# Kernel optimization log

Hardware: AMD Instinct MI355X
Metric: run time of the kernel (lower is better)

## Reference

```python
import jax, jax.numpy as jnp
import numpy as np

EPS = 1e-8  # torch.nn.CosineSimilarity default eps


def setup_inputs() -> dict:
    key = jax.random.key(0)
    ks = jax.random.split(key, 6)
    B, N, SD, HD, AD = 512, 256, 1024, 512, 256
    return {
        "state_emb": jax.random.normal(ks[0], (B, SD), dtype=jnp.float32),
        "hints_emb": jax.random.normal(ks[1], (B, N, HD), dtype=jnp.float32),
        "Ws": jax.random.normal(ks[2], (AD, SD), dtype=jnp.float32) * 0.02,
        "bs": jax.random.normal(ks[3], (AD,), dtype=jnp.float32) * 0.02,
        "Wh": jax.random.normal(ks[4], (AD, HD), dtype=jnp.float32) * 0.02,
        "bh": jax.random.normal(ks[5], (AD,), dtype=jnp.float32) * 0.02,
    }


def reference(state_emb, hints_emb, Ws, bs, Wh, bh):
    # Projections
    sp = state_emb @ Ws.T + bs                       # (B, A)
    hp = jnp.einsum("bnh,ah->bna", hints_emb, Wh) + bh  # (B, N, A)
    # Cosine similarity along feature dim (torch CosineSimilarity semantics)
    sn = jnp.maximum(jnp.linalg.norm(sp, axis=-1, keepdims=True), EPS)    # (B,1)
    hn = jnp.maximum(jnp.linalg.norm(hp, axis=-1), EPS)                   # (B,N)
    scores = jnp.einsum("ba,bna->bn", sp, hp) / (sn * hn)                 # (B,N)
    attn_weights = jax.nn.softmax(scores, axis=1)                         # (B,N)
    # Weighted sum over hints (original, unprojected embeddings)
    output = jnp.einsum("bn,bnh->bh", attn_weights, hints_emb)            # (B,HD)
    return output
```

## Files before the change

### kernel.cpp

```cpp
#include <hip/hip_runtime.h>
#include <hip/hip_bf16.h>

typedef __attribute__((ext_vector_type(8))) short bf16x8;
typedef __attribute__((ext_vector_type(4))) float f32x4;

#define B_  512
#define N_  256
#define SD_ 1024
#define HD_ 512
#define AD_ 256

__device__ __forceinline__ unsigned short f2bf(float f) {
    unsigned int u = __float_as_uint(f);
    unsigned int r = (u + 0x7FFFu + ((u >> 16) & 1u)) >> 16;
    return (unsigned short)r;
}

__global__ void k0_pack(const float* __restrict__ Wh, unsigned short* __restrict__ whp) {
    int g = blockIdx.x * 256 + threadIdx.x;
    int ct  = g >> 10;
    int rem = g & 1023;
    int ks  = rem >> 6;
    int l   = rem & 63;
    int a   = ct * 16 + (l & 15);
    int kb  = ks * 32 + (l >> 4) * 8;
    const float* src = Wh + (size_t)a * HD_ + kb;
    float4 v0 = *(const float4*)(src);
    float4 v1 = *(const float4*)(src + 4);
    bf16x8 o;
    o[0] = (short)f2bf(v0.x); o[1] = (short)f2bf(v0.y);
    o[2] = (short)f2bf(v0.z); o[3] = (short)f2bf(v0.w);
    o[4] = (short)f2bf(v1.x); o[5] = (short)f2bf(v1.y);
    o[6] = (short)f2bf(v1.z); o[7] = (short)f2bf(v1.w);
    ((bf16x8*)whp)[g] = o;
}

__global__ __launch_bounds__(512) void k1_proj(
    const float* __restrict__ state, const float* __restrict__ Ws,
    const float* __restrict__ bs,
    float* __restrict__ sn, float* __restrict__ spv)
{
    __shared__ float st[2][SD_];
    __shared__ float spl[2][AD_];
    __shared__ float red[2][AD_];
    int tid = threadIdx.x, lane = tid & 63, w = tid >> 6;
    int b0 = blockIdx.x * 2;
    ((float4*)st)[tid] = ((const float4*)(state + (size_t)b0 * SD_))[tid];
    __syncthreads();
    float4 s0[4], s1[4];
    #pragma unroll
    for (int seg = 0; seg < 4; ++seg) {
        s0[seg] = *(const float4*)&st[0][seg * 256 + lane * 4];
        s1[seg] = *(const float4*)&st[1][seg * 256 + lane * 4];
    }
    #pragma unroll 2
    for (int i = 0; i < 32; ++i) {
        int a = w * 32 + i;
        const float4* wr = (const float4*)(Ws + (size_t)a * SD_);
        float p0 = 0.f, p1 = 0.f;
        #pragma unroll
        for (int seg = 0; seg < 4; ++seg) {
            float4 wv = wr[seg * 64 + lane];
            p0 += wv.x * s0[seg].x + wv.y * s0[seg].y + wv.z * s0[seg].z + wv.w * s0[seg].w;
            p1 += wv.x * s1[seg].x + wv.y * s1[seg].y + wv.z * s1[seg].z + wv.w * s1[seg].w;
        }
        #pragma unroll
        for (int d = 1; d < 64; d <<= 1) { p0 += __shfl_xor(p0, d); p1 += __shfl_xor(p1, d); }
        if (lane == 0) {
            float bsa = bs[a];
            spl[0][a] = p0 + bsa;
            spl[1][a] = p1 + bsa;
        }
    }
    __syncthreads();
    int tb = tid >> 8, t = tid & 255;
    float sv = spl[tb][t];
    spv[(size_t)(b0 + tb) * AD_ + t] = sv;
    red[tb][t] = sv * sv;
    __syncthreads();
    for (int s = 128; s > 0; s >>= 1) { if (t < s) red[tb][t] += red[tb][t + s]; __syncthreads(); }
    if (t == 0) sn[b0 + tb] = fmaxf(sqrtf(red[tb][0]), 1e-8f);
}

__device__ __forceinline__ void stage_tile(unsigned short* buf, const float4* v,
                                           int rr, int cg) {
    #pragma unroll
    for (int j = 0; j < 4; ++j) {
        int row = j * 16 + rr;
        float4 x = v[j];
        ushort4 u;
        u.x = f2bf(x.x); u.y = f2bf(x.y); u.z = f2bf(x.z); u.w = f2bf(x.w);
        *(ushort4*)((char*)buf + row * 256 + ((cg * 8) ^ ((row & 7) << 4))) = u;
    }
}

__global__ __launch_bounds__(512, 2) void k2_fused(
    const float* __restrict__ hints, const unsigned short* __restrict__ whp,
    const float* __restrict__ spv, const float* __restrict__ sn,
    const float* __restrict__ bh, float* __restrict__ out)
{
    __shared__ __align__(16) char smem[41984];
    unsigned short* A_bf0 = (unsigned short*)smem;
    unsigned short* A_bf1 = (unsigned short*)(smem + 16384);
    float* sp_lds  = (float*)(smem + 32768);
    float* bh_lds  = (float*)(smem + 33792);
    float* norm2p  = (float*)(smem + 34816);
    float* nump    = (float*)(smem + 36864);
    float* sc      = (float*)(smem + 38912);
    float* red     = (float*)(smem + 39936);
    float* wsm     = (float*)(smem + 40960);
    float* scratch = (float*)smem;

    int tid = threadIdx.x, lane = tid & 63, w = tid >> 6;
    int b = blockIdx.x;
    const float* hb = hints + (size_t)b * N_ * HD_;
    if (tid < 64) ((float4*)sp_lds)[tid] = ((const float4*)(spv + (size_t)b * AD_))[tid];
    else if (tid < 128) ((float4*)bh_lds)[tid - 64] = ((const float4*)bh)[tid - 64];
    float snb = sn[b];
    int rr = tid >> 5;
    int cg = tid & 31;
    int cl = lane & 15;
    const float* hrow = hb + (size_t)rr * HD_ + cg * 4;
    __syncthreads();
    float bh0 = bh_lds[(2 * w + 0) * 16 + cl];
    float bh1 = bh_lds[(2 * w + 1) * 16 + cl];
    float sp0 = sp_lds[(2 * w + 0) * 16 + cl];
    float sp1 = sp_lds[(2 * w + 1) * 16 + cl];

    float4 v[4];
    #pragma unroll
    for (int j = 0; j < 4; ++j)
        v[j] = *(const float4*)(hrow + (size_t)(j * 16) * HD_);

    for (int mc = 0; mc < 4; ++mc) {
        f32x4 acc[4][2];
        #pragma unroll
        for (int mf = 0; mf < 4; ++mf) {
            acc[mf][0] = (f32x4){0.f, 0.f, 0.f, 0.f};
            acc[mf][1] = (f32x4){0.f, 0.f, 0.f, 0.f};
        }
        stage_tile(A_bf0, v, rr, cg);
        __syncthreads();

        for (int kc = 0; kc < 4; ++kc) {
            if (kc < 3) {
                #pragma unroll
                for (int j = 0; j < 4; ++j)
                    v[j] = *(const float4*)(hrow + (size_t)(mc * 64 + j * 16) * HD_ + (kc + 1) * 128);
            }
            const unsigned short* Ab = (kc & 1) ? A_bf1 : A_bf0;
            int kc4 = kc * 4;
            #pragma unroll
            for (int ks = 0; ks < 4; ++ks) {
                bf16x8 bfr0 = ((const bf16x8*)whp)[((2 * w + 0) * 16 + kc4 + ks) * 64 + lane];
                bf16x8 bfr1 = ((const bf16x8*)whp)[((2 * w + 1) * 16 + kc4 + ks) * 64 + lane];
                #pragma unroll
                for (int mf = 0; mf < 4; ++mf) {
                    int r = mf * 16 + cl;
                    bf16x8 afr = *(const bf16x8*)((const char*)Ab + r * 256 +
                                 ((ks * 64 + (lane >> 4) * 16) ^ ((r & 7) << 4)));
                    acc[mf][0] = __builtin_amdgcn_mfma_f32_16x16x32_bf16(afr, bfr0, acc[mf][0], 0, 0, 0);
                    acc[mf][1] = __builtin_amdgcn_mfma_f32_16x16x32_bf16(afr, bfr1, acc[mf][1], 0, 0, 0);
                }
            }
            if (kc < 3) stage_tile((kc & 1) ? A_bf0 : A_bf1, v, rr, cg);
            __syncthreads();
        }

        #pragma unroll
        for (int mf = 0; mf < 4; ++mf) {
            #pragma unroll
            for (int r = 0; r < 4; ++r) {
                float h0 = acc[mf][0][r] + bh0;
                float h1 = acc[mf][1][r] + bh1;
                float vv = h0 * h0 + h1 * h1;
                float uu = sp0 * h0 + sp1 * h1;
                vv += __shfl_xor(vv, 1); uu += __shfl_xor(uu, 1);
                vv += __shfl_xor(vv, 2); uu += __shfl_xor(uu, 2);
                vv += __shfl_xor(vv, 4); uu += __shfl_xor(uu, 4);
                vv += __shfl_xor(vv, 8); uu += __shfl_xor(uu, 8);
                if (cl == 0) {
                    int idx = w * 64 + mf * 16 + (lane >> 4) * 4 + r;
                    norm2p[idx] = vv;
                    nump[idx]   = uu;
                }
            }
        }
        if (mc < 3) {
            #pragma unroll
            for (int j = 0; j < 4; ++j)
                v[j] = *(const float4*)(hrow + (size_t)((mc + 1) * 64 + j * 16) * HD_);
        }
        __syncthreads();
        if (tid < 64) {
            float n2 = 0.f, nm = 0.f;
            #pragma unroll
            for (int ww = 0; ww < 8; ++ww) {
                n2 += norm2p[ww * 64 + tid];
                nm += nump[ww * 64 + tid];
            }
            float hn = fmaxf(sqrtf(n2), 1e-8f);
            sc[mc * 64 + tid] = nm / (snb * hn);
        }
        __syncthreads();
    }

    if (tid < 256) red[tid] = sc[tid];
    __syncthreads();
    for (int s = 128; s > 0; s >>= 1) { if (tid < s) red[tid] = fmaxf(red[tid], red[tid + s]); __syncthreads(); }
    float mx = red[0];
    __syncthreads();
    if (tid < 256) { float e = __expf(sc[tid] - mx); sc[tid] = e; red[tid] = e; }
    __syncthreads();
    for (int s = 128; s > 0; s >>= 1) { if (tid < s) red[tid] += red[tid + s]; __syncthreads(); }
    float inv = 1.f / red[0];
    __syncthreads();
    if (tid < 256) wsm[tid] = sc[tid] * inv;
    __syncthreads();

    int hg = tid & 127, ng = tid >> 7;
    const float* hbe = hb + (size_t)(ng * 64) * HD_ + hg * 4;
    float ax = 0.f, ay = 0.f, az = 0.f, aw = 0.f;
    #pragma unroll 8
    for (int n = 0; n < 64; ++n) {
        float4 hv = *(const float4*)(hbe + (size_t)n * HD_);
        float wn = wsm[ng * 64 + n];
        ax += wn * hv.x; ay += wn * hv.y; az += wn * hv.z; aw += wn * hv.w;
    }
    *(float4*)(scratch + ng * 512 + hg * 4) = (float4){ax, ay, az, aw};
    __syncthreads();
    out[(size_t)b * HD_ + tid] =
        scratch[tid] + scratch[512 + tid] + scratch[1024 + tid] + scratch[1536 + tid];
}

extern "C" void kernel_launch(void* const* d_in, const int* in_sizes, int n_in,
                              void* d_out, int out_size, void* d_ws, size_t ws_size,
                              hipStream_t stream) {
    const float* state = (const float*)d_in[0];
    const float* hints = (const float*)d_in[1];
    const float* Ws    = (const float*)d_in[2];
    const float* bs    = (const float*)d_in[3];
    const float* Wh    = (const float*)d_in[4];
    const float* bh    = (const float*)d_in[5];
    float* out = (float*)d_out;

    float* sn = (float*)d_ws;
    float* spv = sn + B_;
    unsigned short* whp = (unsigned short*)(spv + (size_t)B_ * AD_);

    k0_pack<<<64, 256, 0, stream>>>(Wh, whp);
    k1_proj<<<B_ / 2, 512, 0, stream>>>(state, Ws, bs, sn, spv);
    k2_fused<<<B_, 512, 0, stream>>>(hints, whp, spv, sn, bh, out);
}
```

Measured before the change: 153.2 us.

## Triple-buffer LDS tiles with two-stage register prefetch across chunk boundaries

```diff
diff --git a/kernel.cpp b/kernel.cpp
--- a/kernel.cpp
+++ b/kernel.cpp
@@ -90,7 +90,7 @@
         float4 x = v[j];
         ushort4 u;
         u.x = f2bf(x.x); u.y = f2bf(x.y); u.z = f2bf(x.z); u.w = f2bf(x.w);
-        *(ushort4*)((char*)buf + row * 256 + ((cg * 8) ^ ((row & 7) << 4))) = u;
+        *(ushort4*)((char*)buf + row * 256 + ((cg * 8) ^ ((row & 15) << 4))) = u;
     }
 }
 
@@ -99,16 +99,17 @@
     const float* __restrict__ spv, const float* __restrict__ sn,
     const float* __restrict__ bh, float* __restrict__ out)
 {
-    __shared__ __align__(16) char smem[41984];
-    unsigned short* A_bf0 = (unsigned short*)smem;
-    unsigned short* A_bf1 = (unsigned short*)(smem + 16384);
-    float* sp_lds  = (float*)(smem + 32768);
-    float* bh_lds  = (float*)(smem + 33792);
-    float* norm2p  = (float*)(smem + 34816);
-    float* nump    = (float*)(smem + 36864);
-    float* sc      = (float*)(smem + 38912);
-    float* red     = (float*)(smem + 39936);
-    float* wsm     = (float*)(smem + 40960);
+    __shared__ __align__(16) char smem[58368];
+    unsigned short* buf0 = (unsigned short*)smem;
+    unsigned short* buf1 = (unsigned short*)(smem + 16384);
+    unsigned short* buf2 = (unsigned short*)(smem + 32768);
+    float* sp_lds  = (float*)(smem + 49152);
+    float* bh_lds  = (float*)(smem + 50176);
+    float* norm2p  = (float*)(smem + 51200);
+    float* nump    = (float*)(smem + 53248);
+    float* sc      = (float*)(smem + 55296);
+    float* red     = (float*)(smem + 56320);
+    float* wsm     = (float*)(smem + 57344);
     float* scratch = (float*)smem;
 
     int tid = threadIdx.x, lane = tid & 63, w = tid >> 6;
@@ -127,10 +128,16 @@
     float sp0 = sp_lds[(2 * w + 0) * 16 + cl];
     float sp1 = sp_lds[(2 * w + 1) * 16 + cl];
 
-    float4 v[4];
-    #pragma unroll
-    for (int j = 0; j < 4; ++j)
-        v[j] = *(const float4*)(hrow + (size_t)(j * 16) * HD_);
+#define LADDR(p, j) (hrow + (size_t)(((p) >> 2) * 64 + (j) * 16) * HD_ + ((p) & 3) * 128)
+
+    float4 va[4], vb[4];
+    #pragma unroll
+    for (int j = 0; j < 4; ++j) va[j] = *(const float4*)LADDR(0, j);
+    #pragma unroll
+    for (int j = 0; j < 4; ++j) vb[j] = *(const float4*)LADDR(1, j);
+    stage_tile(buf0, va, rr, cg);
+    __syncthreads();
+    unsigned short *bufR = buf0, *bufW = buf1, *bufS = buf2;
 
     for (int mc = 0; mc < 4; ++mc) {
         f32x4 acc[4][2];
@@ -139,32 +146,34 @@
             acc[mf][0] = (f32x4){0.f, 0.f, 0.f, 0.f};
             acc[mf][1] = (f32x4){0.f, 0.f, 0.f, 0.f};
         }
-        stage_tile(A_bf0, v, rr, cg);
-        __syncthreads();
-
+        #pragma unroll
         for (int kc = 0; kc < 4; ++kc) {
-            if (kc < 3) {
-                #pragma unroll
-                for (int j = 0; j < 4; ++j)
-                    v[j] = *(const float4*)(hrow + (size_t)(mc * 64 + j * 16) * HD_ + (kc + 1) * 128);
-            }
-            const unsigned short* Ab = (kc & 1) ? A_bf1 : A_bf0;
-            int kc4 = kc * 4;
+            int p = mc * 4 + kc;
+            if (p + 2 < 16) {
+                if ((kc & 1) == 0) {
+                    #pragma unroll
+                    for (int j = 0; j < 4; ++j) va[j] = *(const float4*)LADDR(p + 2, j);
+                } else {
+                    #pragma unroll
+                    for (int j = 0; j < 4; ++j) vb[j] = *(const float4*)LADDR(p + 2, j);
+                }
+            }
             #pragma unroll
             for (int ks = 0; ks < 4; ++ks) {
-                bf16x8 bfr0 = ((const bf16x8*)whp)[((2 * w + 0) * 16 + kc4 + ks) * 64 + lane];
-                bf16x8 bfr1 = ((const bf16x8*)whp)[((2 * w + 1) * 16 + kc4 + ks) * 64 + lane];
+                bf16x8 bfr0 = ((const bf16x8*)whp)[((2 * w + 0) * 16 + kc * 4 + ks) * 64 + lane];
+                bf16x8 bfr1 = ((const bf16x8*)whp)[((2 * w + 1) * 16 + kc * 4 + ks) * 64 + lane];
                 #pragma unroll
                 for (int mf = 0; mf < 4; ++mf) {
                     int r = mf * 16 + cl;
-                    bf16x8 afr = *(const bf16x8*)((const char*)Ab + r * 256 +
-                                 ((ks * 64 + (lane >> 4) * 16) ^ ((r & 7) << 4)));
+                    bf16x8 afr = *(const bf16x8*)((const char*)bufR + r * 256 +
+                                 ((ks * 64 + (lane >> 4) * 16) ^ ((r & 15) << 4)));
                     acc[mf][0] = __builtin_amdgcn_mfma_f32_16x16x32_bf16(afr, bfr0, acc[mf][0], 0, 0, 0);
                     acc[mf][1] = __builtin_amdgcn_mfma_f32_16x16x32_bf16(afr, bfr1, acc[mf][1], 0, 0, 0);
                 }
             }
-            if (kc < 3) stage_tile((kc & 1) ? A_bf0 : A_bf1, v, rr, cg);
+            if (p + 1 < 16) stage_tile(bufW, (kc & 1) ? va : vb, rr, cg);
             __syncthreads();
+            unsigned short* t0 = bufR; bufR = bufW; bufW = bufS; bufS = t0;
         }
 
         #pragma unroll
@@ -186,11 +195,6 @@
                 }
             }
         }
-        if (mc < 3) {
-            #pragma unroll
-            for (int j = 0; j < 4; ++j)
-                v[j] = *(const float4*)(hrow + (size_t)((mc + 1) * 64 + j * 16) * HD_);
-        }
         __syncthreads();
         if (tid < 64) {
             float n2 = 0.f, nm = 0.f;
@@ -204,6 +208,7 @@
         }
         __syncthreads();
     }
+#undef LADDR
 
     if (tid < 256) red[tid] = sc[tid];
     __syncthreads();
```

New measurement: 147.6 us. 3.7% less time.

## Stage full 64x512 bf16 hint tile per chunk instead of double-buffered K slices

Applied to the files above, without the earlier changes.

```diff
diff --git a/kernel.cpp b/kernel.cpp
--- a/kernel.cpp
+++ b/kernel.cpp
@@ -82,33 +82,20 @@
     if (t == 0) sn[b0 + tb] = fmaxf(sqrtf(red[tb][0]), 1e-8f);
 }
 
-__device__ __forceinline__ void stage_tile(unsigned short* buf, const float4* v,
-                                           int rr, int cg) {
-    #pragma unroll
-    for (int j = 0; j < 4; ++j) {
-        int row = j * 16 + rr;
-        float4 x = v[j];
-        ushort4 u;
-        u.x = f2bf(x.x); u.y = f2bf(x.y); u.z = f2bf(x.z); u.w = f2bf(x.w);
-        *(ushort4*)((char*)buf + row * 256 + ((cg * 8) ^ ((row & 7) << 4))) = u;
-    }
-}
-
 __global__ __launch_bounds__(512, 2) void k2_fused(
     const float* __restrict__ hints, const unsigned short* __restrict__ whp,
     const float* __restrict__ spv, const float* __restrict__ sn,
     const float* __restrict__ bh, float* __restrict__ out)
 {
-    __shared__ __align__(16) char smem[41984];
-    unsigned short* A_bf0 = (unsigned short*)smem;
-    unsigned short* A_bf1 = (unsigned short*)(smem + 16384);
-    float* sp_lds  = (float*)(smem + 32768);
-    float* bh_lds  = (float*)(smem + 33792);
-    float* norm2p  = (float*)(smem + 34816);
-    float* nump    = (float*)(smem + 36864);
-    float* sc      = (float*)(smem + 38912);
-    float* red     = (float*)(smem + 39936);
-    float* wsm     = (float*)(smem + 40960);
+    __shared__ __align__(16) char smem[74752];
+    unsigned short* tile = (unsigned short*)smem;
+    float* sp_lds  = (float*)(smem + 65536);
+    float* bh_lds  = (float*)(smem + 66560);
+    float* norm2p  = (float*)(smem + 67584);
+    float* nump    = (float*)(smem + 69632);
+    float* sc      = (float*)(smem + 71680);
+    float* red     = (float*)(smem + 72704);
+    float* wsm     = (float*)(smem + 73728);
     float* scratch = (float*)smem;
 
     int tid = threadIdx.x, lane = tid & 63, w = tid >> 6;
@@ -117,54 +104,59 @@
     if (tid < 64) ((float4*)sp_lds)[tid] = ((const float4*)(spv + (size_t)b * AD_))[tid];
     else if (tid < 128) ((float4*)bh_lds)[tid - 64] = ((const float4*)bh)[tid - 64];
     float snb = sn[b];
-    int rr = tid >> 5;
-    int cg = tid & 31;
     int cl = lane & 15;
-    const float* hrow = hb + (size_t)rr * HD_ + cg * 4;
+    int srow = tid >> 3;
+    int sseg = tid & 7;
+    const float* srcrow = hb + (size_t)srow * HD_ + sseg * 64;
     __syncthreads();
     float bh0 = bh_lds[(2 * w + 0) * 16 + cl];
     float bh1 = bh_lds[(2 * w + 1) * 16 + cl];
     float sp0 = sp_lds[(2 * w + 0) * 16 + cl];
     float sp1 = sp_lds[(2 * w + 1) * 16 + cl];
 
-    float4 v[4];
-    #pragma unroll
-    for (int j = 0; j < 4; ++j)
-        v[j] = *(const float4*)(hrow + (size_t)(j * 16) * HD_);
-
+    #pragma unroll 1
     for (int mc = 0; mc < 4; ++mc) {
+        const float* src = srcrow + (size_t)(mc * 64) * HD_;
+        #pragma unroll
+        for (int h = 0; h < 2; ++h) {
+            float4 v[8];
+            #pragma unroll
+            for (int j = 0; j < 8; ++j)
+                v[j] = *(const float4*)(src + h * 32 + j * 4);
+            #pragma unroll
+            for (int j2 = 0; j2 < 4; ++j2) {
+                int s = sseg * 8 + h * 4 + j2;
+                int sw = s ^ (srow & 15);
+                float4 a = v[2 * j2], c = v[2 * j2 + 1];
+                bf16x8 pk;
+                pk[0] = (short)f2bf(a.x); pk[1] = (short)f2bf(a.y);
+                pk[2] = (short)f2bf(a.z); pk[3] = (short)f2bf(a.w);
+                pk[4] = (short)f2bf(c.x); pk[5] = (short)f2bf(c.y);
+                pk[6] = (short)f2bf(c.z); pk[7] = (short)f2bf(c.w);
+                *(bf16x8*)((char*)tile + srow * 1024 + sw * 16) = pk;
+            }
+        }
+        __syncthreads();
+
         f32x4 acc[4][2];
         #pragma unroll
         for (int mf = 0; mf < 4; ++mf) {
             acc[mf][0] = (f32x4){0.f, 0.f, 0.f, 0.f};
             acc[mf][1] = (f32x4){0.f, 0.f, 0.f, 0.f};
         }
-        stage_tile(A_bf0, v, rr, cg);
-        __syncthreads();
-
-        for (int kc = 0; kc < 4; ++kc) {
-            if (kc < 3) {
-                #pragma unroll
-                for (int j = 0; j < 4; ++j)
-                    v[j] = *(const float4*)(hrow + (size_t)(mc * 64 + j * 16) * HD_ + (kc + 1) * 128);
-            }
-            const unsigned short* Ab = (kc & 1) ? A_bf1 : A_bf0;
-            int kc4 = kc * 4;
-            #pragma unroll
-            for (int ks = 0; ks < 4; ++ks) {
-                bf16x8 bfr0 = ((const bf16x8*)whp)[((2 * w + 0) * 16 + kc4 + ks) * 64 + lane];
-                bf16x8 bfr1 = ((const bf16x8*)whp)[((2 * w + 1) * 16 + kc4 + ks) * 64 + lane];
-                #pragma unroll
-                for (int mf = 0; mf < 4; ++mf) {
-                    int r = mf * 16 + cl;
-                    bf16x8 afr = *(const bf16x8*)((const char*)Ab + r * 256 +
-                                 ((ks * 64 + (lane >> 4) * 16) ^ ((r & 7) << 4)));
-                    acc[mf][0] = __builtin_amdgcn_mfma_f32_16x16x32_bf16(afr, bfr0, acc[mf][0], 0, 0, 0);
-                    acc[mf][1] = __builtin_amdgcn_mfma_f32_16x16x32_bf16(afr, bfr1, acc[mf][1], 0, 0, 0);
-                }
-            }
-            if (kc < 3) stage_tile((kc & 1) ? A_bf0 : A_bf1, v, rr, cg);
-            __syncthreads();
+        #pragma unroll
+        for (int kidx = 0; kidx < 16; ++kidx) {
+            bf16x8 bfr0 = ((const bf16x8*)whp)[((2 * w + 0) * 16 + kidx) * 64 + lane];
+            bf16x8 bfr1 = ((const bf16x8*)whp)[((2 * w + 1) * 16 + kidx) * 64 + lane];
+            #pragma unroll
+            for (int mf = 0; mf < 4; ++mf) {
+                int r = mf * 16 + cl;
+                int s = kidx * 4 + (lane >> 4);
+                bf16x8 afr = *(const bf16x8*)((const char*)tile + r * 1024 +
+                                              ((s ^ (r & 15)) << 4));
+                acc[mf][0] = __builtin_amdgcn_mfma_f32_16x16x32_bf16(afr, bfr0, acc[mf][0], 0, 0, 0);
+                acc[mf][1] = __builtin_amdgcn_mfma_f32_16x16x32_bf16(afr, bfr1, acc[mf][1], 0, 0, 0);
+            }
         }
 
         #pragma unroll
@@ -186,11 +178,6 @@
                 }
             }
         }
-        if (mc < 3) {
-            #pragma unroll
-            for (int j = 0; j < 4; ++j)
-                v[j] = *(const float4*)(hrow + (size_t)((mc + 1) * 64 + j * 16) * HD_);
-        }
         __syncthreads();
         if (tid < 64) {
             float n2 = 0.f, nm = 0.f;
@@ -202,8 +189,8 @@
             float hn = fmaxf(sqrtf(n2), 1e-8f);
             sc[mc * 64 + tid] = nm / (snb * hn);
         }
-        __syncthreads();
-    }
+    }
+    __syncthreads();
 
     if (tid < 256) red[tid] = sc[tid];
     __syncthreads();
```

After: 165.6 us. +8.1%, slower.
